# Kernel optimization log

Measured on AMD Instinct MI355X. Metric: run time of the kernel, lower is better.

Reference implementation:

```python
import jax, jax.numpy as jnp
import numpy as np

C, P, H, W, BS = 256, 2, 128, 128, 4
NH, DH = 16, 16
NPATCH = (H // P) * (W // P)   # 4096
NTOK = NPATCH + 1              # 4097 with cls token
NMASK = int((1 - 0.75) * NTOK) # 1024 kept (visible) tokens
PRED = 512
NUM_BLOCKS = 1

def _sincos_pos_embed(embed_dim, h, w):
    # faithful port of get_2d_sincos_pos_embed
    def emb1d(d, pos):
        omega = np.arange(d // 2, dtype=np.float64) / (d / 2.0)
        omega = 1.0 / 10000 ** omega
        out = np.einsum('m,d->md', pos.reshape(-1), omega)
        return np.concatenate([np.sin(out), np.cos(out)], axis=1)
    gh = np.arange(h, dtype=np.float32)
    gw = np.arange(w, dtype=np.float32)
    grid = np.stack(np.meshgrid(gw, gh), axis=0).reshape(2, 1, h, w)
    emb = np.concatenate([emb1d(embed_dim // 2, grid[0]), emb1d(embed_dim // 2, grid[1])], axis=1)
    return jnp.asarray(emb, jnp.float32)  # [h*w, embed_dim]

def _ln(x, g, b, eps=1e-5):
    mu = x.mean(-1, keepdims=True)
    var = ((x - mu) ** 2).mean(-1, keepdims=True)
    return (x - mu) * jax.lax.rsqrt(var + eps) * g + b

def _gelu(x):
    return jax.nn.gelu(x, approximate=False)  # torch nn.GELU default (erf)

def _attn(x, qkv_w, qkv_b, proj_w, proj_b, nq_g, nq_b, nk_g, nk_b):
    bs, n, c = x.shape
    qkv = x @ qkv_w + qkv_b
    q, k, v = jnp.split(qkv, 3, axis=-1)
    heads = lambda t: t.reshape(bs, n, NH, DH).transpose(0, 2, 1, 3)  # [b,h,n,d]
    q, k, v = heads(q), heads(k), heads(v)
    q = _ln(q, nq_g, nq_b)  # per-head-dim QK LayerNorm
    k = _ln(k, nk_g, nk_b)
    score = jnp.einsum('bhnd,bhmd->bhnm', q, k) / np.float32(np.sqrt(DH))
    attn = jax.nn.softmax(score, axis=-1)
    attn_map = attn.mean(axis=1)[:, 0, 1:]  # [b, n-1]
    out = jnp.einsum('bhnm,bhmd->bhnd', attn, v)
    out = out.transpose(0, 2, 1, 3).reshape(bs, n, c)
    return out @ proj_w + proj_b, attn_map

def _forward(mask_index, x, Wp, bp, cls, qkv_w, qkv_b, proj_w, proj_b, nq_g, nq_b, nk_g, nk_b,
             conv_w, conv_b, ca1_w, ca1_b, ca2_w, ca2_b, mlp1_w, mlp1_b, mlp2_w, mlp2_b,
             node_w, ln0_g, ln0_b, h1_w, h1_b, ln1_g, ln1_b, h2_w, h2_b, ln2_g, ln2_b,
             h3_w, h3_b, pr_w, pr_b):
    bs = x.shape[0]
    # PatchEmbed: conv stride=kernel=P expressed as reshape + einsum
    xp = x.reshape(bs, 3, H // P, P, W // P, P)
    tok = jnp.einsum('bchpwq,ocpq->bohw', xp, Wp) + bp[None, :, None, None]
    tok = tok.reshape(bs, C, NPATCH).transpose(0, 2, 1)  # [b, l, c]
    tok = tok + _sincos_pos_embed(C, H // P, W // P)[None]
    tok = jnp.concatenate([jnp.broadcast_to(cls, (bs, 1, C)), tok], axis=1)  # prepend cls
    # mask_img: keep NMASK tokens per the precomputed permutation prefix
    m = jnp.take_along_axis(tok, mask_index[:, :, None], axis=1)  # [b, NMASK, C]

    attn_map = None
    for blk in range(NUM_BLOCKS):
        feat = m[..., None]  # feature_list: [b, l, c, width]
        for i in range(4):
            j = blk * 4 + i
            xl = feat[..., -1]
            o1 = _gelu(xl @ conv_w[j] + conv_b[j])  # Conv1x1Act
            gate = jax.nn.sigmoid(jax.nn.relu(xl @ ca1_w[j] + ca1_b[j]) @ ca2_w[j] + ca2_b[j])
            o2 = gate * xl                           # ChannelAttention
            o4 = _gelu(xl @ mlp1_w[j] + mlp1_b[j]) @ mlp2_w[j] + mlp2_b[j]  # MLP
            cat = jnp.concatenate([feat, jnp.stack([o1, o2, xl, o4], axis=-1)], axis=-1)  # width 5+i
            wmix = jax.nn.softmax(node_w[j, :5 + i] / 0.01)
            mixed = jnp.einsum('blcn,n->blc', cat, wmix)
            a_out, attn_map = _attn(mixed, qkv_w[j], qkv_b[j], proj_w[j], proj_b[j],
                                    nq_g[j], nq_b[j], nk_g[j], nk_b[j])
            xo = a_out + mixed  # residual
            feat = jnp.concatenate([feat, xo[..., None]], axis=-1)
        m = xo
    # Predict_head (tokenwise)
    h = _ln(m, ln0_g, ln0_b)
    h = h @ h1_w + h1_b
    h = _ln(h, ln1_g, ln1_b)
    h = h @ h2_w + h2_b
    h = _ln(h, ln2_g, ln2_b)
    h = h @ h3_w + h3_b
    return h @ pr_w + pr_b  # [b, NMASK, PRED]

def setup_inputs():
    key = jax.random.key(0)
    ks = iter(jax.random.split(key, 64))
    rn = lambda shape, s=0.02: jax.random.normal(next(ks), shape, jnp.float32) * s
    noise = jax.random.normal(next(ks), (BS, NTOK))
    mask_index = jnp.argsort(noise, axis=-1)[:, :NMASK].astype(jnp.int32)
    return dict(
        x=jax.random.normal(next(ks), (BS, 3, H, W), jnp.float32),
        mask_index=mask_index,
        Wp=rn((C, 3, P, P)), bp=jnp.zeros((C,)), cls=rn((1, 1, C)),
        qkv_w=rn((4, C, 3 * C)), qkv_b=jnp.zeros((4, 3 * C)),
        proj_w=rn((4, C, C)), proj_b=jnp.zeros((4, C)),
        nq_g=jnp.ones((4, DH)), nq_b=jnp.zeros((4, DH)),
        nk_g=jnp.ones((4, DH)), nk_b=jnp.zeros((4, DH)),
        conv_w=rn((4, C, C)), conv_b=jnp.zeros((4, C)),
        ca1_w=rn((4, C, C // 16)), ca1_b=jnp.zeros((4, C // 16)),
        ca2_w=rn((4, C // 16, C)), ca2_b=jnp.zeros((4, C)),
        mlp1_w=rn((4, C, 4 * C)), mlp1_b=jnp.zeros((4, 4 * C)),
        mlp2_w=rn((4, 4 * C, C)), mlp2_b=jnp.zeros((4, C)),
        node_w=jax.random.normal(next(ks), (4, 8), jnp.float32),
        ln0_g=jnp.ones((C,)), ln0_b=jnp.zeros((C,)),
        h1_w=rn((C, 2048)), h1_b=jnp.zeros((2048,)),
        ln1_g=jnp.ones((2048,)), ln1_b=jnp.zeros((2048,)),
        h2_w=rn((2048, 256)), h2_b=jnp.zeros((256,)),
        ln2_g=jnp.ones((256,)), ln2_b=jnp.zeros((256,)),
        h3_w=rn((256, 2048)), h3_b=jnp.zeros((2048,)),
        pr_w=rn((2048, PRED)), pr_b=jnp.zeros((PRED,)),
    )

def reference(x, mask_index, Wp, bp, cls, qkv_w, qkv_b, proj_w, proj_b, nq_g, nq_b, nk_g, nk_b,
              conv_w, conv_b, ca1_w, ca1_b, ca2_w, ca2_b, mlp1_w, mlp1_b, mlp2_w, mlp2_b,
              node_w, ln0_g, ln0_b, h1_w, h1_b, ln1_g, ln1_b, h2_w, h2_b, ln2_g, ln2_b,
              h3_w, h3_b, pr_w, pr_b):
    return _forward(mask_index, x, Wp, bp, cls, qkv_w, qkv_b, proj_w, proj_b, nq_g, nq_b, nk_g, nk_b,
                    conv_w, conv_b, ca1_w, ca1_b, ca2_w, ca2_b, mlp1_w, mlp1_b, mlp2_w, mlp2_b,
                    node_w, ln0_g, ln0_b, h1_w, h1_b, ln1_g, ln1_b, h2_w, h2_b, ln2_g, ln2_b,
                    h3_w, h3_b, pr_w, pr_b)
```

## Files before the change

kernel.cpp:

```cpp
#include <hip/hip_runtime.h>
#include <math.h>
#include <cstddef>

#define RTOK 4096
#define CDIM 256
#define NHEAD 16
#define DHEAD 16
#define SEQ 1024
#define BSZ 4

#define ACT_NONE 0
#define ACT_GELU 1

typedef short short8 __attribute__((ext_vector_type(8)));
typedef float f32x4  __attribute__((ext_vector_type(4)));
typedef _Float16 half8 __attribute__((ext_vector_type(8)));
typedef _Float16 half4 __attribute__((ext_vector_type(4)));

__device__ __forceinline__ float gelu_erf(float x) {
    return 0.5f * x * (1.0f + erff(x * 0.70710678118654752f));
}
__device__ __forceinline__ unsigned short f2b(float f) {
    unsigned u = __float_as_uint(f);
    unsigned r = (u + 0x7FFFu + ((u >> 16) & 1u)) >> 16;
    return (unsigned short)r;
}
__device__ __forceinline__ float b2f(unsigned short u) {
    return __uint_as_float((unsigned)u << 16);
}
__device__ __forceinline__ void gld16(const unsigned short* g, unsigned short* l) {
    __builtin_amdgcn_global_load_lds(
        (const __attribute__((address_space(1))) unsigned int*)g,
        (__attribute__((address_space(3))) unsigned int*)l, 16, 0, 0);
}

struct WtSeg { const float* in; unsigned short* out; int K, N, ntx, tpz, zin, zout; };
struct WtTab { WtSeg s[9]; int cum[10]; };

__global__ __launch_bounds__(256) void wtrans_all(WtTab tab)
{
    int g = blockIdx.x;
    int si = 0;
    #pragma unroll
    for (int i = 0; i < 8; ++i) if (g >= tab.cum[i + 1]) si = i + 1;
    WtSeg sg = tab.s[si];
    int t = g - tab.cum[si];
    int z = t / sg.tpz, r = t % sg.tpz;
    int kb = (r % sg.ntx) * 32, nb = (r / sg.ntx) * 32;
    const float* in = sg.in + (size_t)z * sg.zin;
    unsigned short* out = sg.out + (size_t)z * sg.zout;

    __shared__ float tt[32][33];
    int tx = threadIdx.x & 31, ty = threadIdx.x >> 5;
    #pragma unroll
    for (int rr = 0; rr < 4; ++rr) {
        int kk = ty * 4 + rr;
        tt[kk][tx] = in[(size_t)(kb + kk) * sg.N + nb + tx];
    }
    __syncthreads();
    #pragma unroll
    for (int rr = 0; rr < 4; ++rr) {
        int nn = ty * 4 + rr;
        out[(size_t)(nb + nn) * sg.K + kb + tx] = f2b(tt[tx][nn]);
    }
}

__global__ __launch_bounds__(256) void embed_kernel(
    const float* __restrict__ x, const int* __restrict__ mask_index,
    const float* __restrict__ Wp, const float* __restrict__ bp,
    const float* __restrict__ cls,
    float* __restrict__ out, unsigned short* __restrict__ outb)
{
    int row = blockIdx.x;
    int b = row >> 10;
    int c = threadIdx.x;
    int idx = mask_index[row];
    if (idx == 0) {
        float v = cls[c];
        out[(size_t)row * 256 + c] = v;
        outb[(size_t)row * 256 + c] = f2b(v);
        return;
    }
    int p  = idx - 1;
    int ph = p >> 6, pw = p & 63;

    __shared__ float xs[12];
    if (c < 12) {
        int ch = c >> 2, r = (c >> 1) & 1, q = c & 1;
        xs[c] = x[(((size_t)b * 3 + ch) * 128 + (ph * 2 + r)) * 128 + (pw * 2 + q)];
    }
    __syncthreads();

    float acc = bp[c];
    #pragma unroll
    for (int t = 0; t < 12; ++t) acc += xs[t] * Wp[c * 12 + t];

    int part = c >> 6, cc = c & 63;
    double omega = exp((double)cc * -0.14391156831212787);
    double posv  = (part < 2) ? (double)pw : (double)ph;
    double a     = posv * omega;
    double e     = ((part & 1) == 0) ? sin(a) : cos(a);
    float v = acc + (float)e;
    out[(size_t)row * 256 + c] = v;
    outb[(size_t)row * 256 + c] = f2b(v);
}

template<int MT, int ACT, bool RES, bool FOUT, int BMODE, bool SPLIT>
__global__ __launch_bounds__(256) void gemm_mfma(
    const unsigned short* __restrict__ A, const unsigned short* __restrict__ Bt,
    const float* __restrict__ bias, const float* __restrict__ bias1,
    const float* __restrict__ Rsd,
    float* __restrict__ C, unsigned short* __restrict__ Cb,
    int M, int N, int K, int N0)
{
    constexpr int BM = 64 * MT;
    __shared__ __align__(16) unsigned short As[BM * 64];
    __shared__ __align__(16) unsigned short Bs[64 * 64];
    int tid = threadIdx.x;
    int w = tid >> 6, lane = tid & 63;
    int l15 = lane & 15, q = lane >> 4;

    int gx = gridDim.x, gy = gridDim.y;
    int L = blockIdx.x + gx * blockIdx.y;
    int xcd = L & 7, j = L >> 3;
    int by = xcd * (gy >> 3) + j / gx;
    int bx = j - (j / gx) * gx;
    int row0 = by * BM, col0 = bx * 64;

    f32x4 acc[MT][4];
    #pragma unroll
    for (int mt = 0; mt < MT; ++mt)
        #pragma unroll
        for (int nt = 0; nt < 4; ++nt)
            acc[mt][nt] = (f32x4){0.f, 0.f, 0.f, 0.f};

    for (int kb = 0; kb < K; kb += 64) {
        __syncthreads();
        #pragma unroll
        for (int t = 0; t < 2 * MT; ++t) {
            int slot = tid + t * 256;
            int r = slot >> 3;
            int s = (slot & 7) ^ (r & 7);
            gld16(A + (size_t)(row0 + r) * K + kb + s * 8, &As[slot * 8]);
        }
        #pragma unroll
        for (int t = 0; t < 2; ++t) {
            int slot = tid + t * 256;
            int r = slot >> 3;
            int s = (slot & 7) ^ (r & 7);
            gld16(Bt + (size_t)(col0 + r) * K + kb + s * 8, &Bs[slot * 8]);
        }
        __syncthreads();

        #pragma unroll
        for (int hh = 0; hh < 2; ++hh) {
            short8 af[MT];
            #pragma unroll
            for (int mt = 0; mt < MT; ++mt) {
                int R = w * 16 * MT + mt * 16 + l15;
                int c = hh * 4 + q;
                af[mt] = *(const short8*)&As[R * 64 + ((c ^ (R & 7)) << 3)];
            }
            #pragma unroll
            for (int nt = 0; nt < 4; ++nt) {
                int R = nt * 16 + l15;
                int c = hh * 4 + q;
                short8 bf = *(const short8*)&Bs[R * 64 + ((c ^ (R & 7)) << 3)];
                #pragma unroll
                for (int mt = 0; mt < MT; ++mt)
                    acc[mt][nt] = __builtin_amdgcn_mfma_f32_16x16x32_bf16(
                        af[mt], bf, acc[mt][nt], 0, 0, 0);
            }
        }
    }

    #pragma unroll
    for (int mt = 0; mt < MT; ++mt) {
        #pragma unroll
        for (int nt = 0; nt < 4; ++nt) {
            #pragma unroll
            for (int reg = 0; reg < 4; ++reg) {
                int row = row0 + w * 16 * MT + mt * 16 + q * 4 + reg;
                int col = col0 + nt * 16 + l15;
                if (SPLIT) {
                    float v = acc[mt][nt][reg] +
                              (col < N0 ? bias[col] : bias1[col - N0]);
                    if (ACT == ACT_GELU) v = gelu_erf(v);
                    if (col < N0) C[(size_t)row * N0 + col] = v;
                    else Cb[(size_t)row * (N - N0) + (col - N0)] = f2b(v);
                } else {
                    float v = acc[mt][nt][reg] + bias[col];
                    if (ACT == ACT_GELU) v = gelu_erf(v);
                    if (RES) v += Rsd[(size_t)row * N + col];
                    if (FOUT) C[(size_t)row * N + col] = v;
                    if (BMODE == 1) Cb[(size_t)row * N + col] = f2b(v);
                    if (BMODE == 2) {
                        _Float16 hv = (_Float16)v;
                        Cb[(size_t)row * N + col] = *(unsigned short*)&hv;
                    }
                }
            }
        }
    }
}

__global__ __launch_bounds__(256) void chanattn_kernel(
    const float* __restrict__ xl, const float* __restrict__ ca1w,
    const float* __restrict__ ca1b, const float* __restrict__ ca2w,
    const float* __restrict__ ca2b, float* __restrict__ o2)
{
    __shared__ float xs[256];
    __shared__ float sm16[16];
    size_t row = blockIdx.x;
    int tid = threadIdx.x;
    xs[tid] = xl[row * 256 + tid];
    __syncthreads();

    int h = tid >> 4, part = tid & 15;
    float p = 0.f;
    #pragma unroll
    for (int i = 0; i < 16; ++i)
        p += xs[part * 16 + i] * ca1w[(part * 16 + i) * 16 + h];
    p += __shfl_down(p, 8, 16);
    p += __shfl_down(p, 4, 16);
    p += __shfl_down(p, 2, 16);
    p += __shfl_down(p, 1, 16);
    if (part == 0) sm16[h] = fmaxf(p + ca1b[h], 0.0f);
    __syncthreads();

    float g = ca2b[tid];
    #pragma unroll
    for (int hh = 0; hh < 16; ++hh) g += sm16[hh] * ca2w[hh * 256 + tid];
    g = 1.0f / (1.0f + expf(-g));
    o2[row * 256 + tid] = g * xs[tid];
}

__global__ __launch_bounds__(256) void mix_kernel(
    const float* p0, const float* p1, const float* p2, const float* p3,
    const float* p4, const float* p5, const float* p6, const float* p7,
    const float* __restrict__ node_w, int cnt,
    float* __restrict__ out, unsigned short* __restrict__ outb, int n)
{
    int i = blockIdx.x * 256 + threadIdx.x;
    if (i >= n) return;
    float w[8];
    float mx = -1e30f;
    for (int t = 0; t < cnt; ++t) { w[t] = node_w[t] * 100.0f; mx = fmaxf(mx, w[t]); }
    float s = 0.0f;
    for (int t = 0; t < cnt; ++t) { w[t] = expf(w[t] - mx); s += w[t]; }
    float inv = 1.0f / s;
    const float* ps[8] = {p0, p1, p2, p3, p4, p5, p6, p7};
    float v = 0.0f;
    for (int t = 0; t < cnt; ++t) v += w[t] * inv * ps[t][i];
    out[i] = v;
    outb[i] = f2b(v);
}

__global__ __launch_bounds__(256) void ln256_kernel(
    const float* __restrict__ in, unsigned short* __restrict__ outb,
    const float* __restrict__ g, const float* __restrict__ bb)
{
    int row = blockIdx.x * 4 + (threadIdx.x >> 6);
    int lane = threadIdx.x & 63;
    f32x4 xv = *(const f32x4*)(in + (size_t)row * 256 + lane * 4);
    float s = xv[0] + xv[1] + xv[2] + xv[3];
    #pragma unroll
    for (int off = 1; off < 64; off <<= 1) s += __shfl_xor(s, off, 64);
    float mu = s * (1.0f / 256.0f);
    float d0 = xv[0]-mu, d1 = xv[1]-mu, d2 = xv[2]-mu, d3 = xv[3]-mu;
    float s2 = d0*d0 + d1*d1 + d2*d2 + d3*d3;
    #pragma unroll
    for (int off = 1; off < 64; off <<= 1) s2 += __shfl_xor(s2, off, 64);
    float rstd = rsqrtf(s2 * (1.0f / 256.0f) + 1e-5f);
    f32x4 gv = *(const f32x4*)(g + lane * 4);
    f32x4 bv = *(const f32x4*)(bb + lane * 4);
    ushort4 o;
    o.x = f2b(d0 * rstd * gv[0] + bv[0]);
    o.y = f2b(d1 * rstd * gv[1] + bv[1]);
    o.z = f2b(d2 * rstd * gv[2] + bv[2]);
    o.w = f2b(d3 * rstd * gv[3] + bv[3]);
    *(ushort4*)(outb + (size_t)row * 256 + lane * 4) = o;
}

__global__ __launch_bounds__(256) void lnwb_kernel(
    const unsigned short* __restrict__ in, unsigned short* __restrict__ outb,
    const float* __restrict__ g, const float* __restrict__ bb, int N)
{
    __shared__ float sm[4];
    size_t row = blockIdx.x;
    const unsigned short* xr = in + row * N;
    int lane = threadIdx.x & 63, wid = threadIdx.x >> 6;

    float s = 0.0f;
    for (int i = threadIdx.x; i < N; i += 256) s += b2f(xr[i]);
    #pragma unroll
    for (int off = 32; off > 0; off >>= 1) s += __shfl_down(s, off, 64);
    if (lane == 0) sm[wid] = s;
    __syncthreads();
    float mu = (sm[0] + sm[1] + sm[2] + sm[3]) / N;
    __syncthreads();

    float s2 = 0.0f;
    for (int i = threadIdx.x; i < N; i += 256) { float d = b2f(xr[i]) - mu; s2 += d * d; }
    #pragma unroll
    for (int off = 32; off > 0; off >>= 1) s2 += __shfl_down(s2, off, 64);
    if (lane == 0) sm[wid] = s2;
    __syncthreads();
    float var = (sm[0] + sm[1] + sm[2] + sm[3]) / N;
    float rstd = rsqrtf(var + 1e-5f);

    for (int i = threadIdx.x; i < N; i += 256)
        outb[row * N + i] = f2b((b2f(xr[i]) - mu) * rstd * g[i] + bb[i]);
}

__global__ __launch_bounds__(256) void attn_kernel(
    const unsigned short* __restrict__ qkvh,
    const float* __restrict__ nqg, const float* __restrict__ nqb,
    const float* __restrict__ nkg, const float* __restrict__ nkb,
    unsigned short* __restrict__ outb)
{
    int qt = blockIdx.x, h = blockIdx.y, b = blockIdx.z;
    int tid = threadIdx.x;
    int w = tid >> 6, lane = tid & 63;
    int l15 = lane & 15, quad = lane >> 4;
    const _Float16* qkv = (const _Float16*)qkvh;

    __shared__ __align__(16) _Float16 Qs[128 * 40];
    __shared__ __align__(16) _Float16 Kb[128 * 40];
    __shared__ __align__(16) _Float16 Vt[16 * 136];
    __shared__ __align__(16) _Float16 Ps[4][16 * 136];

    const float QSC = 0.25f * 1.44269504088896340736f;

    if (tid < 128) {
        int r = tid;
        const _Float16* qp = qkv + ((size_t)(b * 1024 + qt * 128 + r)) * 768 + h * 16;
        half8 a0 = *(const half8*)(qp);
        half8 a1 = *(const half8*)(qp + 8);
        float v[16];
        #pragma unroll
        for (int e = 0; e < 8; ++e) { v[e] = (float)a0[e]; v[8 + e] = (float)a1[e]; }
        float mu = 0.f;
        #pragma unroll
        for (int d = 0; d < 16; ++d) mu += v[d];
        mu *= (1.0f / 16.0f);
        float var = 0.f;
        #pragma unroll
        for (int d = 0; d < 16; ++d) { float t = v[d] - mu; var += t * t; }
        var *= (1.0f / 16.0f);
        float rstd = rsqrtf(var + 1e-5f);
        #pragma unroll
        for (int d4 = 0; d4 < 4; ++d4) {
            half4 t;
            #pragma unroll
            for (int e = 0; e < 4; ++e)
                t[e] = (_Float16)(((v[d4*4+e] - mu) * rstd * nqg[d4*4+e] + nqb[d4*4+e]) * QSC);
            *(half4*)&Qs[r * 40 + d4 * 4] = t;
        }
        half4 z = (half4){(_Float16)0, (_Float16)0, (_Float16)0, (_Float16)0};
        #pragma unroll
        for (int d4 = 4; d4 < 8; ++d4) {
            *(half4*)&Qs[r * 40 + d4 * 4] = z;
            *(half4*)&Kb[r * 40 + d4 * 4] = z;
        }
    }
    __syncthreads();

    half8 bq[2];
    bq[0] = *(const half8*)&Qs[(w * 32 + l15) * 40 + quad * 8];
    bq[1] = *(const half8*)&Qs[(w * 32 + 16 + l15) * 40 + quad * 8];

    float mst[2] = {-1e30f, -1e30f};
    float lst[2] = {0.f, 0.f};
    f32x4 acco[2];
    acco[0] = (f32x4){0.f, 0.f, 0.f, 0.f};
    acco[1] = (f32x4){0.f, 0.f, 0.f, 0.f};

    for (int kt = 0; kt < 8; ++kt) {
        __syncthreads();
        if (tid < 128) {
            int r = tid;
            const _Float16* kp = qkv + ((size_t)(b * 1024 + kt * 128 + r)) * 768 + 256 + h * 16;
            half8 a0 = *(const half8*)(kp);
            half8 a1 = *(const half8*)(kp + 8);
            float v[16];
            #pragma unroll
            for (int e = 0; e < 8; ++e) { v[e] = (float)a0[e]; v[8 + e] = (float)a1[e]; }
            float mu = 0.f;
            #pragma unroll
            for (int d = 0; d < 16; ++d) mu += v[d];
            mu *= (1.0f / 16.0f);
            float var = 0.f;
            #pragma unroll
            for (int d = 0; d < 16; ++d) { float t = v[d] - mu; var += t * t; }
            var *= (1.0f / 16.0f);
            float rstd = rsqrtf(var + 1e-5f);
            #pragma unroll
            for (int d4 = 0; d4 < 4; ++d4) {
                half4 t;
                #pragma unroll
                for (int e = 0; e < 4; ++e)
                    t[e] = (_Float16)((v[d4*4+e] - mu) * rstd * nkg[d4*4+e] + nkb[d4*4+e]);
                *(half4*)&Kb[r * 40 + d4 * 4] = t;
            }
        } else {
            int r = tid - 128;
            const _Float16* vp = qkv + ((size_t)(b * 1024 + kt * 128 + r)) * 768 + 512 + h * 16;
            half8 a0 = *(const half8*)(vp);
            half8 a1 = *(const half8*)(vp + 8);
            #pragma unroll
            for (int e = 0; e < 8; ++e) {
                Vt[e * 136 + r] = a0[e];
                Vt[(8 + e) * 136 + r] = a1[e];
            }
        }
        __syncthreads();

        f32x4 sacc[2][8];
        #pragma unroll
        for (int ni = 0; ni < 8; ++ni) {
            half8 ak = *(const half8*)&Kb[(ni * 16 + l15) * 40 + quad * 8];
            sacc[0][ni] = __builtin_amdgcn_mfma_f32_16x16x32_f16(
                ak, bq[0], (f32x4){0.f, 0.f, 0.f, 0.f}, 0, 0, 0);
            sacc[1][ni] = __builtin_amdgcn_mfma_f32_16x16x32_f16(
                ak, bq[1], (f32x4){0.f, 0.f, 0.f, 0.f}, 0, 0, 0);
        }

        half8 bv[4];
        #pragma unroll
        for (int c = 0; c < 4; ++c)
            bv[c] = *(const half8*)&Vt[l15 * 136 + c * 32 + quad * 8];

        #pragma unroll
        for (int mi = 0; mi < 2; ++mi) {
            float rm = sacc[mi][0][0];
            #pragma unroll
            for (int ni = 0; ni < 8; ++ni)
                #pragma unroll
                for (int reg = 0; reg < 4; ++reg)
                    rm = fmaxf(rm, sacc[mi][ni][reg]);
            rm = fmaxf(rm, __shfl_xor(rm, 16, 64));
            rm = fmaxf(rm, __shfl_xor(rm, 32, 64));
            float mn  = fmaxf(mst[mi], rm);
            float cor = exp2f(mst[mi] - mn);
            mst[mi] = mn;
            lst[mi] *= cor;
            #pragma unroll
            for (int reg = 0; reg < 4; ++reg) {
                float cR = __shfl(cor, (lane & 48) + quad * 4 + reg, 64);
                acco[mi][reg] *= cR;
            }
            float lsum = 0.f;
            #pragma unroll
            for (int ni = 0; ni < 8; ++ni) {
                half4 ph;
                #pragma unroll
                for (int reg = 0; reg < 4; ++reg) {
                    float p = exp2f(sacc[mi][ni][reg] - mn);
                    lsum += p;
                    ph[reg] = (_Float16)p;
                }
                *(half4*)&Ps[w][l15 * 136 + ni * 16 + quad * 4] = ph;
            }
            lsum += __shfl_xor(lsum, 16, 64);
            lsum += __shfl_xor(lsum, 32, 64);
            lst[mi] += lsum;

            #pragma unroll
            for (int c = 0; c < 4; ++c) {
                half8 p0 = *(const half8*)&Ps[w][l15 * 136 + c * 32 + quad * 8];
                acco[mi] = __builtin_amdgcn_mfma_f32_16x16x32_f16(p0, bv[c], acco[mi], 0, 0, 0);
            }
        }
    }

    #pragma unroll
    for (int mi = 0; mi < 2; ++mi) {
        #pragma unroll
        for (int reg = 0; reg < 4; ++reg) {
            float lR = __shfl(lst[mi], (lane & 48) + quad * 4 + reg, 64);
            float o = acco[mi][reg] / lR;
            int row = b * 1024 + qt * 128 + w * 32 + mi * 16 + quad * 4 + reg;
            outb[(size_t)row * 256 + h * 16 + l15] = f2b(o);
        }
    }
}

extern "C" void kernel_launch(void* const* d_in, const int* in_sizes, int n_in,
                              void* d_out, int out_size, void* d_ws, size_t ws_size,
                              hipStream_t stream)
{
    const float* x          = (const float*)d_in[0];
    const int*   mask_index = (const int*)  d_in[1];
    const float* Wp         = (const float*)d_in[2];
    const float* bp         = (const float*)d_in[3];
    const float* cls        = (const float*)d_in[4];
    const float* qkv_w      = (const float*)d_in[5];
    const float* qkv_b      = (const float*)d_in[6];
    const float* proj_w     = (const float*)d_in[7];
    const float* proj_b     = (const float*)d_in[8];
    const float* nq_g       = (const float*)d_in[9];
    const float* nq_b       = (const float*)d_in[10];
    const float* nk_g       = (const float*)d_in[11];
    const float* nk_b       = (const float*)d_in[12];
    const float* conv_w     = (const float*)d_in[13];
    const float* conv_b     = (const float*)d_in[14];
    const float* ca1_w      = (const float*)d_in[15];
    const float* ca1_b      = (const float*)d_in[16];
    const float* ca2_w      = (const float*)d_in[17];
    const float* ca2_b      = (const float*)d_in[18];
    const float* mlp1_w     = (const float*)d_in[19];
    const float* mlp1_b     = (const float*)d_in[20];
    const float* mlp2_w     = (const float*)d_in[21];
    const float* mlp2_b     = (const float*)d_in[22];
    const float* node_w     = (const float*)d_in[23];
    const float* ln0_g      = (const float*)d_in[24];
    const float* ln0_b      = (const float*)d_in[25];
    const float* h1_w       = (const float*)d_in[26];
    const float* h1_b       = (const float*)d_in[27];
    const float* ln1_g      = (const float*)d_in[28];
    const float* ln1_b      = (const float*)d_in[29];
    const float* h2_w       = (const float*)d_in[30];
    const float* h2_b       = (const float*)d_in[31];
    const float* ln2_g      = (const float*)d_in[32];
    const float* ln2_b      = (const float*)d_in[33];
    const float* h3_w       = (const float*)d_in[34];
    const float* h3_b       = (const float*)d_in[35];
    const float* pr_w       = (const float*)d_in[36];
    const float* pr_b       = (const float*)d_in[37];
    float* out = (float*)d_out;

    char* base = (char*)d_ws;
    size_t off = 0;
    auto alloc = [&](size_t bytes) -> char* {
        char* p = base + off;
        off += (bytes + 255) & ~(size_t)255;
        return p;
    };
    const size_t RC = (size_t)RTOK * CDIM;
    float* F[5];
    unsigned short* Fb[5];
    for (int i = 0; i < 5; ++i) F[i] = (float*)alloc(RC * 4);
    for (int i = 0; i < 5; ++i) Fb[i] = (unsigned short*)alloc(RC * 2);
    float* O1  = (float*)alloc(RC * 4);
    float* O2  = (float*)alloc(RC * 4);
    float* O4  = (float*)alloc(RC * 4);
    float* MIX = (float*)alloc(RC * 4);
    unsigned short* MIXb = (unsigned short*)alloc(RC * 2);
    unsigned short* AOb  = (unsigned short*)alloc(RC * 2);
    unsigned short* BIGH = (unsigned short*)alloc((size_t)RTOK * 768 * 2);
    unsigned short* H1b  = (unsigned short*)alloc((size_t)RTOK * 2048 * 2);
    unsigned short* MIDU = (unsigned short*)alloc((size_t)RTOK * 2048 * 2);
    unsigned short* L0b  = (unsigned short*)alloc(RC * 2);
    unsigned short* L2b  = (unsigned short*)alloc(RC * 2);
    unsigned short* H3b  = (unsigned short*)alloc((size_t)RTOK * 2048 * 2);
    unsigned short* cm1b  = (unsigned short*)alloc((size_t)4 * 1280 * 256 * 2);
    unsigned short* qkvb  = (unsigned short*)alloc((size_t)4 * 768 * 256 * 2);
    unsigned short* projb = (unsigned short*)alloc((size_t)4 * 256 * 256 * 2);
    unsigned short* mlp2b = (unsigned short*)alloc((size_t)4 * 256 * 1024 * 2);
    unsigned short* h1b   = (unsigned short*)alloc((size_t)2048 * 256 * 2);
    unsigned short* h2b   = (unsigned short*)alloc((size_t)256 * 2048 * 2);
    unsigned short* h3b   = (unsigned short*)alloc((size_t)2048 * 256 * 2);
    unsigned short* prb   = (unsigned short*)alloc((size_t)512 * 2048 * 2);

    {
        WtTab tab;
        int c = 0, idx = 0;
        auto seg = [&](const float* in, unsigned short* outp, int K, int N,
                       int z, int zin, int zout) {
            WtSeg s; s.in = in; s.out = outp; s.K = K; s.N = N;
            s.ntx = K / 32; s.tpz = (K / 32) * (N / 32);
            s.zin = zin; s.zout = zout;
            tab.s[idx] = s; tab.cum[idx] = c;
            c += s.tpz * z; ++idx;
        };
        seg(conv_w, cm1b,         256, 256,  4, 256 * 256,  1280 * 256);
        seg(mlp1_w, cm1b + 65536, 256, 1024, 4, 256 * 1024, 1280 * 256);
        seg(qkv_w,  qkvb,  256, 768,  4, 256 * 768,  768 * 256);
        seg(proj_w, projb, 256, 256,  4, 256 * 256,  256 * 256);
        seg(mlp2_w, mlp2b, 1024, 256, 4, 1024 * 256, 256 * 1024);
        seg(h1_w, h1b, 256, 2048, 1, 0, 0);
        seg(h2_w, h2b, 2048, 256, 1, 0, 0);
        seg(h3_w, h3b, 256, 2048, 1, 0, 0);
        seg(pr_w, prb, 2048, 512, 1, 0, 0);
        tab.cum[9] = c;
        wtrans_all<<<c, 256, 0, stream>>>(tab);
    }

    embed_kernel<<<RTOK, 256, 0, stream>>>(x, mask_index, Wp, bp, cls, F[0], Fb[0]);

    for (int j = 0; j < 4; ++j) {
        const float* xl = F[j];
        const unsigned short* xlb = Fb[j];
        gemm_mfma<2, ACT_GELU, false, false, 0, true><<<dim3(20, 32), 256, 0, stream>>>(
            xlb, cm1b + (size_t)j * 1280 * 256, conv_b + j * 256, mlp1_b + j * 1024,
            nullptr, O1, MIDU, RTOK, 1280, 256, 256);
        chanattn_kernel<<<RTOK, 256, 0, stream>>>(
            xl, ca1_w + (size_t)j * 256 * 16, ca1_b + j * 16,
            ca2_w + (size_t)j * 16 * 256, ca2_b + j * 256, O2);
        gemm_mfma<1, ACT_NONE, false, true, 0, false><<<dim3(4, 64), 256, 0, stream>>>(
            MIDU, mlp2b + (size_t)j * 256 * 1024, mlp2_b + j * 256, nullptr, nullptr,
            O4, nullptr, RTOK, 256, 1024, 0);
        const float* ps[8] = {nullptr, nullptr, nullptr, nullptr,
                              nullptr, nullptr, nullptr, nullptr};
        int cnt = 0;
        for (int t = 0; t <= j; ++t) ps[cnt++] = F[t];
        ps[cnt++] = O1; ps[cnt++] = O2; ps[cnt++] = F[j]; ps[cnt++] = O4;
        mix_kernel<<<(int)(RC / 256), 256, 0, stream>>>(
            ps[0], ps[1], ps[2], ps[3], ps[4], ps[5], ps[6], ps[7],
            node_w + j * 8, cnt, MIX, MIXb, (int)RC);
        gemm_mfma<2, ACT_NONE, false, false, 2, false><<<dim3(12, 32), 256, 0, stream>>>(
            MIXb, qkvb + (size_t)j * 768 * 256, qkv_b + j * 768, nullptr, nullptr,
            nullptr, BIGH, RTOK, 768, 256, 0);
        attn_kernel<<<dim3(8, NHEAD, BSZ), 256, 0, stream>>>(
            BIGH, nq_g + j * 16, nq_b + j * 16, nk_g + j * 16, nk_b + j * 16, AOb);
        gemm_mfma<1, ACT_NONE, true, true, 1, false><<<dim3(4, 64), 256, 0, stream>>>(
            AOb, projb + (size_t)j * 256 * 256, proj_b + j * 256, nullptr, MIX,
            F[j + 1], Fb[j + 1], RTOK, 256, 256, 0);
    }

    ln256_kernel<<<1024, 256, 0, stream>>>(F[4], L0b, ln0_g, ln0_b);
    gemm_mfma<2, ACT_NONE, false, false, 1, false><<<dim3(32, 32), 256, 0, stream>>>(
        L0b, h1b, h1_b, nullptr, nullptr, nullptr, H1b, RTOK, 2048, 256, 0);
    lnwb_kernel<<<RTOK, 256, 0, stream>>>(H1b, MIDU, ln1_g, ln1_b, 2048);
    gemm_mfma<1, ACT_NONE, false, true, 0, false><<<dim3(4, 64), 256, 0, stream>>>(
        MIDU, h2b, h2_b, nullptr, nullptr, MIX, nullptr, RTOK, 256, 2048, 0);
    ln256_kernel<<<1024, 256, 0, stream>>>(MIX, L2b, ln2_g, ln2_b);
    gemm_mfma<2, ACT_NONE, false, false, 1, false><<<dim3(32, 32), 256, 0, stream>>>(
        L2b, h3b, h3_b, nullptr, nullptr, nullptr, H3b, RTOK, 2048, 256, 0);
    gemm_mfma<1, ACT_NONE, false, true, 0, false><<<dim3(8, 64), 256, 0, stream>>>(
        H3b, prb, pr_b, nullptr, nullptr, out, nullptr, RTOK, 512, 2048, 0);
}
```

Measured before the change: 735.7 us.

## Fuse node-weighted mixing into GEMM epilogues and split attention preprocessing

```diff
diff --git a/kernel.cpp b/kernel.cpp
--- a/kernel.cpp
+++ b/kernel.cpp
@@ -32,6 +32,14 @@
     __builtin_amdgcn_global_load_lds(
         (const __attribute__((address_space(1))) unsigned int*)g,
         (__attribute__((address_space(3))) unsigned int*)l, 16, 0, 0);
+}
+__device__ __forceinline__ float node_wsel(const float* nwp, int cnt, int widx) {
+    float ww[8];
+    float mx = -1e30f;
+    for (int t = 0; t < cnt; ++t) { ww[t] = nwp[t] * 100.0f; mx = fmaxf(mx, ww[t]); }
+    float ssum = 0.0f;
+    for (int t = 0; t < cnt; ++t) { ww[t] = expf(ww[t] - mx); ssum += ww[t]; }
+    return ww[widx] / ssum;
 }
 
 struct WtSeg { const float* in; unsigned short* out; int K, N, ntx, tpz, zin, zout; };
@@ -105,13 +113,14 @@
     outb[(size_t)row * 256 + c] = f2b(v);
 }
 
-template<int MT, int ACT, bool RES, bool FOUT, int BMODE, bool SPLIT>
+template<int MT, int ACT, bool RES, bool FOUT, int BMODE, bool SPLIT, int NW>
 __global__ __launch_bounds__(256) void gemm_mfma(
     const unsigned short* __restrict__ A, const unsigned short* __restrict__ Bt,
     const float* __restrict__ bias, const float* __restrict__ bias1,
     const float* __restrict__ Rsd,
     float* __restrict__ C, unsigned short* __restrict__ Cb,
-    int M, int N, int K, int N0)
+    int M, int N, int K, int N0,
+    const float* __restrict__ nwp, int ncnt, int widx)
 {
     constexpr int BM = 64 * MT;
     __shared__ __align__(16) unsigned short As[BM * 64];
@@ -174,6 +183,9 @@
         }
     }
 
+    float wsel = 0.0f;
+    if (NW > 0) wsel = node_wsel(nwp, ncnt, widx);
+
     #pragma unroll
     for (int mt = 0; mt < MT; ++mt) {
         #pragma unroll
@@ -186,12 +198,17 @@
                     float v = acc[mt][nt][reg] +
                               (col < N0 ? bias[col] : bias1[col - N0]);
                     if (ACT == ACT_GELU) v = gelu_erf(v);
-                    if (col < N0) C[(size_t)row * N0 + col] = v;
-                    else Cb[(size_t)row * (N - N0) + (col - N0)] = f2b(v);
+                    if (col < N0) {
+                        if (NW == 1) C[(size_t)row * N0 + col] += wsel * v;
+                        else         C[(size_t)row * N0 + col] = v;
+                    } else {
+                        Cb[(size_t)row * (N - N0) + (col - N0)] = f2b(v);
+                    }
                 } else {
                     float v = acc[mt][nt][reg] + bias[col];
                     if (ACT == ACT_GELU) v = gelu_erf(v);
-                    if (RES) v += Rsd[(size_t)row * N + col];
+                    if (NW == 2) v = wsel * v + Rsd[(size_t)row * N + col];
+                    else if (RES) v += Rsd[(size_t)row * N + col];
                     if (FOUT) C[(size_t)row * N + col] = v;
                     if (BMODE == 1) Cb[(size_t)row * N + col] = f2b(v);
                     if (BMODE == 2) {
@@ -205,9 +222,12 @@
 }
 
 __global__ __launch_bounds__(256) void chanattn_kernel(
-    const float* __restrict__ xl, const float* __restrict__ ca1w,
-    const float* __restrict__ ca1b, const float* __restrict__ ca2w,
-    const float* __restrict__ ca2b, float* __restrict__ o2)
+    const float* __restrict__ xl,
+    const float* f0, const float* f1, const float* f2,
+    const float* __restrict__ ca1w, const float* __restrict__ ca1b,
+    const float* __restrict__ ca2w, const float* __restrict__ ca2b,
+    const float* __restrict__ node_w, int cnt,
+    float* __restrict__ MIX)
 {
     __shared__ float xs[256];
     __shared__ float sm16[16];
@@ -232,28 +252,19 @@
     #pragma unroll
     for (int hh = 0; hh < 16; ++hh) g += sm16[hh] * ca2w[hh * 256 + tid];
     g = 1.0f / (1.0f + expf(-g));
-    o2[row * 256 + tid] = g * xs[tid];
-}
-
-__global__ __launch_bounds__(256) void mix_kernel(
-    const float* p0, const float* p1, const float* p2, const float* p3,
-    const float* p4, const float* p5, const float* p6, const float* p7,
-    const float* __restrict__ node_w, int cnt,
-    float* __restrict__ out, unsigned short* __restrict__ outb, int n)
-{
-    int i = blockIdx.x * 256 + threadIdx.x;
-    if (i >= n) return;
-    float w[8];
+    float o2 = g * xs[tid];
+
+    float ww[8];
     float mx = -1e30f;
-    for (int t = 0; t < cnt; ++t) { w[t] = node_w[t] * 100.0f; mx = fmaxf(mx, w[t]); }
-    float s = 0.0f;
-    for (int t = 0; t < cnt; ++t) { w[t] = expf(w[t] - mx); s += w[t]; }
-    float inv = 1.0f / s;
-    const float* ps[8] = {p0, p1, p2, p3, p4, p5, p6, p7};
-    float v = 0.0f;
-    for (int t = 0; t < cnt; ++t) v += w[t] * inv * ps[t][i];
-    out[i] = v;
-    outb[i] = f2b(v);
+    for (int t = 0; t < cnt; ++t) { ww[t] = node_w[t] * 100.0f; mx = fmaxf(mx, ww[t]); }
+    float ssum = 0.0f;
+    for (int t = 0; t < cnt; ++t) { ww[t] = expf(ww[t] - mx); ssum += ww[t]; }
+    float inv = 1.0f / ssum;
+    int j = cnt - 5;
+    float acc = (ww[j] + ww[j + 3]) * inv * xs[tid] + ww[j + 2] * inv * o2;
+    const float* fs[3] = {f0, f1, f2};
+    for (int t = 0; t < j; ++t) acc += ww[t] * inv * fs[t][row * 256 + tid];
+    MIX[row * 256 + tid] = acc;
 }
 
 __global__ __launch_bounds__(256) void ln256_kernel(
@@ -313,176 +324,206 @@
         outb[row * N + i] = f2b((b2f(xr[i]) - mu) * rstd * g[i] + bb[i]);
 }
 
-__global__ __launch_bounds__(256) void attn_kernel(
+__global__ __launch_bounds__(256) void attn_prep(
     const unsigned short* __restrict__ qkvh,
     const float* __restrict__ nqg, const float* __restrict__ nqb,
     const float* __restrict__ nkg, const float* __restrict__ nkb,
+    unsigned short* __restrict__ Qph, unsigned short* __restrict__ Kph,
+    unsigned short* __restrict__ Vph)
+{
+    int b = blockIdx.x >> 6;
+    int tokbase = (blockIdx.x & 63) * 16;
+    int tid = threadIdx.x;
+    int tl = tid >> 4, h = tid & 15;
+    int tok = tokbase + tl;
+    const _Float16* qkv = (const _Float16*)qkvh;
+    const _Float16* rowp = qkv + ((size_t)(b * 1024 + tok)) * 768;
+    _Float16* Qp = (_Float16*)Qph;
+    _Float16* Kp = (_Float16*)Kph;
+    _Float16* Vp = (_Float16*)Vph;
+    const float QSC = 0.25f * 1.44269504088896340736f;
+
+    __shared__ _Float16 vt[16][16][17];
+
+    {
+        half8 a0 = *(const half8*)(rowp + h * 16);
+        half8 a1 = *(const half8*)(rowp + h * 16 + 8);
+        float v[16];
+        #pragma unroll
+        for (int e = 0; e < 8; ++e) { v[e] = (float)a0[e]; v[8 + e] = (float)a1[e]; }
+        float mu = 0.f;
+        #pragma unroll
+        for (int d = 0; d < 16; ++d) mu += v[d];
+        mu *= (1.0f / 16.0f);
+        float var = 0.f;
+        #pragma unroll
+        for (int d = 0; d < 16; ++d) { float t = v[d] - mu; var += t * t; }
+        var *= (1.0f / 16.0f);
+        float rstd = rsqrtf(var + 1e-5f);
+        half8 o0, o1;
+        #pragma unroll
+        for (int e = 0; e < 8; ++e) {
+            o0[e] = (_Float16)(((v[e] - mu) * rstd * nqg[e] + nqb[e]) * QSC);
+            o1[e] = (_Float16)(((v[8+e] - mu) * rstd * nqg[8+e] + nqb[8+e]) * QSC);
+        }
+        _Float16* qo = Qp + ((size_t)(b * 16 + h) * 1024 + tok) * 16;
+        *(half8*)qo = o0;
+        *(half8*)(qo + 8) = o1;
+    }
+    {
+        half8 a0 = *(const half8*)(rowp + 256 + h * 16);
+        half8 a1 = *(const half8*)(rowp + 256 + h * 16 + 8);
+        float v[16];
+        #pragma unroll
+        for (int e = 0; e < 8; ++e) { v[e] = (float)a0[e]; v[8 + e] = (float)a1[e]; }
+        float mu = 0.f;
+        #pragma unroll
+        for (int d = 0; d < 16; ++d) mu += v[d];
+        mu *= (1.0f / 16.0f);
+        float var = 0.f;
+        #pragma unroll
+        for (int d = 0; d < 16; ++d) { float t = v[d] - mu; var += t * t; }
+        var *= (1.0f / 16.0f);
+        float rstd = rsqrtf(var + 1e-5f);
+        half8 o0, o1;
+        #pragma unroll
+        for (int e = 0; e < 8; ++e) {
+            o0[e] = (_Float16)((v[e] - mu) * rstd * nkg[e] + nkb[e]);
+            o1[e] = (_Float16)((v[8+e] - mu) * rstd * nkg[8+e] + nkb[8+e]);
+        }
+        _Float16* ko = Kp + ((size_t)(b * 16 + h) * 1024 + tok) * 16;
+        *(half8*)ko = o0;
+        *(half8*)(ko + 8) = o1;
+    }
+    {
+        half8 a0 = *(const half8*)(rowp + 512 + h * 16);
+        half8 a1 = *(const half8*)(rowp + 512 + h * 16 + 8);
+        #pragma unroll
+        for (int e = 0; e < 8; ++e) { vt[tl][h][e] = a0[e]; vt[tl][h][8 + e] = a1[e]; }
+    }
+    __syncthreads();
+    {
+        int h2 = tid >> 4, d = tid & 15;
+        half8 o0, o1;
+        #pragma unroll
+        for (int t = 0; t < 8; ++t) { o0[t] = vt[t][h2][d]; o1[t] = vt[8 + t][h2][d]; }
+        _Float16* vo = Vp + ((size_t)(b * 16 + h2) * 16 + d) * 1024 + tokbase;
+        *(half8*)vo = o0;
+        *(half8*)(vo + 8) = o1;
+    }
+}
+
+__global__ __launch_bounds__(256) void attn_kernel(
+    const unsigned short* __restrict__ Qph, const unsigned short* __restrict__ Kph,
+    const unsigned short* __restrict__ Vph,
     unsigned short* __restrict__ outb)
 {
     int qt = blockIdx.x, h = blockIdx.y, b = blockIdx.z;
+    int bh = b * 16 + h;
     int tid = threadIdx.x;
     int w = tid >> 6, lane = tid & 63;
     int l15 = lane & 15, quad = lane >> 4;
-    const _Float16* qkv = (const _Float16*)qkvh;
-
-    __shared__ __align__(16) _Float16 Qs[128 * 40];
+    const _Float16* Qp = (const _Float16*)Qph + (size_t)bh * 1024 * 16;
+    const _Float16* Kp = (const _Float16*)Kph + (size_t)bh * 1024 * 16;
+    const _Float16* Vp = (const _Float16*)Vph + (size_t)bh * 16 * 1024;
+
+    __shared__ __align__(16) _Float16 Qs[64 * 40];
     __shared__ __align__(16) _Float16 Kb[128 * 40];
     __shared__ __align__(16) _Float16 Vt[16 * 136];
     __shared__ __align__(16) _Float16 Ps[4][16 * 136];
 
-    const float QSC = 0.25f * 1.44269504088896340736f;
-
+    uint4 z4 = {0, 0, 0, 0};
+    if (tid < 64) {
+        *(uint4*)&Qs[tid * 40 + 16] = z4;
+        *(uint4*)&Qs[tid * 40 + 24] = z4;
+    } else if (tid < 192) {
+        int r = tid - 64;
+        *(uint4*)&Kb[r * 40 + 16] = z4;
+        *(uint4*)&Kb[r * 40 + 24] = z4;
+    }
     if (tid < 128) {
-        int r = tid;
-        const _Float16* qp = qkv + ((size_t)(b * 1024 + qt * 128 + r)) * 768 + h * 16;
-        half8 a0 = *(const half8*)(qp);
-        half8 a1 = *(const half8*)(qp + 8);
-        float v[16];
-        #pragma unroll
-        for (int e = 0; e < 8; ++e) { v[e] = (float)a0[e]; v[8 + e] = (float)a1[e]; }
-        float mu = 0.f;
-        #pragma unroll
-        for (int d = 0; d < 16; ++d) mu += v[d];
-        mu *= (1.0f / 16.0f);
-        float var = 0.f;
-        #pragma unroll
-        for (int d = 0; d < 16; ++d) { float t = v[d] - mu; var += t * t; }
-        var *= (1.0f / 16.0f);
-        float rstd = rsqrtf(var + 1e-5f);
-        #pragma unroll
-        for (int d4 = 0; d4 < 4; ++d4) {
-            half4 t;
-            #pragma unroll
-            for (int e = 0; e < 4; ++e)
-                t[e] = (_Float16)(((v[d4*4+e] - mu) * rstd * nqg[d4*4+e] + nqb[d4*4+e]) * QSC);
-            *(half4*)&Qs[r * 40 + d4 * 4] = t;
-        }
-        half4 z = (half4){(_Float16)0, (_Float16)0, (_Float16)0, (_Float16)0};
-        #pragma unroll
-        for (int d4 = 4; d4 < 8; ++d4) {
-            *(half4*)&Qs[r * 40 + d4 * 4] = z;
-            *(half4*)&Kb[r * 40 + d4 * 4] = z;
-        }
-    }
-    __syncthreads();
-
-    half8 bq[2];
-    bq[0] = *(const half8*)&Qs[(w * 32 + l15) * 40 + quad * 8];
-    bq[1] = *(const half8*)&Qs[(w * 32 + 16 + l15) * 40 + quad * 8];
-
-    float mst[2] = {-1e30f, -1e30f};
-    float lst[2] = {0.f, 0.f};
-    f32x4 acco[2];
-    acco[0] = (f32x4){0.f, 0.f, 0.f, 0.f};
-    acco[1] = (f32x4){0.f, 0.f, 0.f, 0.f};
+        int r = tid >> 1, part = tid & 1;
+        *(uint4*)&Qs[r * 40 + part * 8] =
+            *(const uint4*)(Qp + (size_t)(qt * 64 + r) * 16 + part * 8);
+    }
+    __syncthreads();
+
+    half8 bq = *(const half8*)&Qs[(w * 16 + l15) * 40 + quad * 8];
+    float mst = -1e30f, lst = 0.f;
+    f32x4 acco = (f32x4){0.f, 0.f, 0.f, 0.f};
 
     for (int kt = 0; kt < 8; ++kt) {
         __syncthreads();
-        if (tid < 128) {
-            int r = tid;
-            const _Float16* kp = qkv + ((size_t)(b * 1024 + kt * 128 + r)) * 768 + 256 + h * 16;
-            half8 a0 = *(const half8*)(kp);
-            half8 a1 = *(const half8*)(kp + 8);
-            float v[16];
-            #pragma unroll
-            for (int e = 0; e < 8; ++e) { v[e] = (float)a0[e]; v[8 + e] = (float)a1[e]; }
-            float mu = 0.f;
-            #pragma unroll
-            for (int d = 0; d < 16; ++d) mu += v[d];
-            mu *= (1.0f / 16.0f);
-            float var = 0.f;
-            #pragma unroll
-            for (int d = 0; d < 16; ++d) { float t = v[d] - mu; var += t * t; }
-            var *= (1.0f / 16.0f);
-            float rstd = rsqrtf(var + 1e-5f);
-            #pragma unroll
-            for (int d4 = 0; d4 < 4; ++d4) {
-                half4 t;
-                #pragma unroll
-                for (int e = 0; e < 4; ++e)
-                    t[e] = (_Float16)((v[d4*4+e] - mu) * rstd * nkg[d4*4+e] + nkb[d4*4+e]);
-                *(half4*)&Kb[r * 40 + d4 * 4] = t;
-            }
-        } else {
-            int r = tid - 128;
-            const _Float16* vp = qkv + ((size_t)(b * 1024 + kt * 128 + r)) * 768 + 512 + h * 16;
-            half8 a0 = *(const half8*)(vp);
-            half8 a1 = *(const half8*)(vp + 8);
-            #pragma unroll
-            for (int e = 0; e < 8; ++e) {
-                Vt[e * 136 + r] = a0[e];
-                Vt[(8 + e) * 136 + r] = a1[e];
-            }
+        {
+            int r = tid >> 1, part = tid & 1;
+            *(uint4*)&Kb[r * 40 + part * 8] =
+                *(const uint4*)(Kp + (size_t)(kt * 128 + r) * 16 + part * 8);
+        }
+        {
+            int d = tid >> 4, kk8 = tid & 15;
+            *(uint4*)&Vt[d * 136 + kk8 * 8] =
+                *(const uint4*)(Vp + (size_t)d * 1024 + kt * 128 + kk8 * 8);
         }
         __syncthreads();
 
-        f32x4 sacc[2][8];
+        f32x4 sacc[8];
         #pragma unroll
         for (int ni = 0; ni < 8; ++ni) {
             half8 ak = *(const half8*)&Kb[(ni * 16 + l15) * 40 + quad * 8];
-            sacc[0][ni] = __builtin_amdgcn_mfma_f32_16x16x32_f16(
-                ak, bq[0], (f32x4){0.f, 0.f, 0.f, 0.f}, 0, 0, 0);
-            sacc[1][ni] = __builtin_amdgcn_mfma_f32_16x16x32_f16(
-                ak, bq[1], (f32x4){0.f, 0.f, 0.f, 0.f}, 0, 0, 0);
-        }
-
+            sacc[ni] = __builtin_amdgcn_mfma_f32_16x16x32_f16(
+                ak, bq, (f32x4){0.f, 0.f, 0.f, 0.f}, 0, 0, 0);
+        }
         half8 bv[4];
         #pragma unroll
         for (int c = 0; c < 4; ++c)
             bv[c] = *(const half8*)&Vt[l15 * 136 + c * 32 + quad * 8];
 
-        #pragma unroll
-        for (int mi = 0; mi < 2; ++mi) {
-            float rm = sacc[mi][0][0];
+        float rm = sacc[0][0];
+        #pragma unroll
+        for (int ni = 0; ni < 8; ++ni)
             #pragma unroll
-            for (int ni = 0; ni < 8; ++ni)
-                #pragma unroll
-                for (int reg = 0; reg < 4; ++reg)
-                    rm = fmaxf(rm, sacc[mi][ni][reg]);
-            rm = fmaxf(rm, __shfl_xor(rm, 16, 64));
-            rm = fmaxf(rm, __shfl_xor(rm, 32, 64));
-            float mn  = fmaxf(mst[mi], rm);
-            float cor = exp2f(mst[mi] - mn);
-            mst[mi] = mn;
-            lst[mi] *= cor;
+            for (int reg = 0; reg < 4; ++reg)
+                rm = fmaxf(rm, sacc[ni][reg]);
+        rm = fmaxf(rm, __shfl_xor(rm, 16, 64));
+        rm = fmaxf(rm, __shfl_xor(rm, 32, 64));
+        float mn  = fmaxf(mst, rm);
+        float cor = exp2f(mst - mn);
+        mst = mn;
+        lst *= cor;
+        #pragma unroll
+        for (int reg = 0; reg < 4; ++reg) {
+            float cR = __shfl(cor, (lane & 48) + quad * 4 + reg, 64);
+            acco[reg] *= cR;
+        }
+        float lsum = 0.f;
+        #pragma unroll
+        for (int ni = 0; ni < 8; ++ni) {
+            half4 ph;
             #pragma unroll
             for (int reg = 0; reg < 4; ++reg) {
-                float cR = __shfl(cor, (lane & 48) + quad * 4 + reg, 64);
-                acco[mi][reg] *= cR;
+                float p = exp2f(sacc[ni][reg] - mn);
+                lsum += p;
+                ph[reg] = (_Float16)p;
             }
-            float lsum = 0.f;
-            #pragma unroll
-            for (int ni = 0; ni < 8; ++ni) {
-                half4 ph;
-                #pragma unroll
-                for (int reg = 0; reg < 4; ++reg) {
-                    float p = exp2f(sacc[mi][ni][reg] - mn);
-                    lsum += p;
-                    ph[reg] = (_Float16)p;
-                }
-                *(half4*)&Ps[w][l15 * 136 + ni * 16 + quad * 4] = ph;
-            }
-            lsum += __shfl_xor(lsum, 16, 64);
-            lsum += __shfl_xor(lsum, 32, 64);
-            lst[mi] += lsum;
-
-            #pragma unroll
-            for (int c = 0; c < 4; ++c) {
-                half8 p0 = *(const half8*)&Ps[w][l15 * 136 + c * 32 + quad * 8];
-                acco[mi] = __builtin_amdgcn_mfma_f32_16x16x32_f16(p0, bv[c], acco[mi], 0, 0, 0);
-            }
-        }
-    }
-
-    #pragma unroll
-    for (int mi = 0; mi < 2; ++mi) {
-        #pragma unroll
-        for (int reg = 0; reg < 4; ++reg) {
-            float lR = __shfl(lst[mi], (lane & 48) + quad * 4 + reg, 64);
-            float o = acco[mi][reg] / lR;
-            int row = b * 1024 + qt * 128 + w * 32 + mi * 16 + quad * 4 + reg;
-            outb[(size_t)row * 256 + h * 16 + l15] = f2b(o);
-        }
+            *(half4*)&Ps[w][l15 * 136 + ni * 16 + quad * 4] = ph;
+        }
+        lsum += __shfl_xor(lsum, 16, 64);
+        lsum += __shfl_xor(lsum, 32, 64);
+        lst += lsum;
+
+        #pragma unroll
+        for (int c = 0; c < 4; ++c) {
+            half8 p0 = *(const half8*)&Ps[w][l15 * 136 + c * 32 + quad * 8];
+            acco = __builtin_amdgcn_mfma_f32_16x16x32_f16(p0, bv[c], acco, 0, 0, 0);
+        }
+    }
+
+    #pragma unroll
+    for (int reg = 0; reg < 4; ++reg) {
+        float lR = __shfl(lst, (lane & 48) + quad * 4 + reg, 64);
+        float o = acco[reg] / lR;
+        int row = b * 1024 + qt * 64 + w * 16 + quad * 4 + reg;
+        outb[(size_t)row * 256 + h * 16 + l15] = f2b(o);
     }
 }
 
@@ -542,13 +583,13 @@
     unsigned short* Fb[5];
     for (int i = 0; i < 5; ++i) F[i] = (float*)alloc(RC * 4);
     for (int i = 0; i < 5; ++i) Fb[i] = (unsigned short*)alloc(RC * 2);
-    float* O1  = (float*)alloc(RC * 4);
-    float* O2  = (float*)alloc(RC * 4);
-    float* O4  = (float*)alloc(RC * 4);
     float* MIX = (float*)alloc(RC * 4);
     unsigned short* MIXb = (unsigned short*)alloc(RC * 2);
     unsigned short* AOb  = (unsigned short*)alloc(RC * 2);
     unsigned short* BIGH = (unsigned short*)alloc((size_t)RTOK * 768 * 2);
+    unsigned short* Qp   = (unsigned short*)alloc((size_t)RTOK * 256 * 2);
+    unsigned short* Kp   = (unsigned short*)alloc((size_t)RTOK * 256 * 2);
+    unsigned short* Vp   = (unsigned short*)alloc((size_t)RTOK * 256 * 2);
     unsigned short* H1b  = (unsigned short*)alloc((size_t)RTOK * 2048 * 2);
     unsigned short* MIDU = (unsigned short*)alloc((size_t)RTOK * 2048 * 2);
     unsigned short* L0b  = (unsigned short*)alloc(RC * 2);
@@ -592,42 +633,42 @@
     for (int j = 0; j < 4; ++j) {
         const float* xl = F[j];
         const unsigned short* xlb = Fb[j];
-        gemm_mfma<2, ACT_GELU, false, false, 0, true><<<dim3(20, 32), 256, 0, stream>>>(
+        chanattn_kernel<<<RTOK, 256, 0, stream>>>(
+            xl, F[0], F[1], F[2],
+            ca1_w + (size_t)j * 256 * 16, ca1_b + j * 16,
+            ca2_w + (size_t)j * 16 * 256, ca2_b + j * 256,
+            node_w + j * 8, 5 + j, MIX);
+        gemm_mfma<2, ACT_GELU, false, false, 0, true, 1><<<dim3(20, 32), 256, 0, stream>>>(
             xlb, cm1b + (size_t)j * 1280 * 256, conv_b + j * 256, mlp1_b + j * 1024,
-            nullptr, O1, MIDU, RTOK, 1280, 256, 256);
-        chanattn_kernel<<<RTOK, 256, 0, stream>>>(
-            xl, ca1_w + (size_t)j * 256 * 16, ca1_b + j * 16,
-            ca2_w + (size_t)j * 16 * 256, ca2_b + j * 256, O2);
-        gemm_mfma<1, ACT_NONE, false, true, 0, false><<<dim3(4, 64), 256, 0, stream>>>(
-            MIDU, mlp2b + (size_t)j * 256 * 1024, mlp2_b + j * 256, nullptr, nullptr,
-            O4, nullptr, RTOK, 256, 1024, 0);
-        const float* ps[8] = {nullptr, nullptr, nullptr, nullptr,
-                              nullptr, nullptr, nullptr, nullptr};
-        int cnt = 0;
-        for (int t = 0; t <= j; ++t) ps[cnt++] = F[t];
-        ps[cnt++] = O1; ps[cnt++] = O2; ps[cnt++] = F[j]; ps[cnt++] = O4;
-        mix_kernel<<<(int)(RC / 256), 256, 0, stream>>>(
-            ps[0], ps[1], ps[2], ps[3], ps[4], ps[5], ps[6], ps[7],
-            node_w + j * 8, cnt, MIX, MIXb, (int)RC);
-        gemm_mfma<2, ACT_NONE, false, false, 2, false><<<dim3(12, 32), 256, 0, stream>>>(
+            nullptr, MIX, MIDU, RTOK, 1280, 256, 256, node_w + j * 8, 5 + j, j + 1);
+        gemm_mfma<1, ACT_NONE, false, true, 1, false, 2><<<dim3(4, 64), 256, 0, stream>>>(
+            MIDU, mlp2b + (size_t)j * 256 * 1024, mlp2_b + j * 256, nullptr, MIX,
+            MIX, MIXb, RTOK, 256, 1024, 0, node_w + j * 8, 5 + j, j + 4);
+        gemm_mfma<2, ACT_NONE, false, false, 2, false, 0><<<dim3(12, 32), 256, 0, stream>>>(
             MIXb, qkvb + (size_t)j * 768 * 256, qkv_b + j * 768, nullptr, nullptr,
-            nullptr, BIGH, RTOK, 768, 256, 0);
-        attn_kernel<<<dim3(8, NHEAD, BSZ), 256, 0, stream>>>(
-            BIGH, nq_g + j * 16, nq_b + j * 16, nk_g + j * 16, nk_b + j * 16, AOb);
-        gemm_mfma<1, ACT_NONE, true, true, 1, false><<<dim3(4, 64), 256, 0, stream>>>(
+            nullptr, BIGH, RTOK, 768, 256, 0, nullptr, 0, 0);
+        attn_prep<<<256, 256, 0, stream>>>(
+            BIGH, nq_g + j * 16, nq_b + j * 16, nk_g + j * 16, nk_b + j * 16,
+            Qp, Kp, Vp);
+        attn_kernel<<<dim3(16, NHEAD, BSZ), 256, 0, stream>>>(Qp, Kp, Vp, AOb);
+        gemm_mfma<1, ACT_NONE, true, true, 1, false, 0><<<dim3(4, 64), 256, 0, stream>>>(
             AOb, projb + (size_t)j * 256 * 256, proj_b + j * 256, nullptr, MIX,
-            F[j + 1], Fb[j + 1], RTOK, 256, 256, 0);
+            F[j + 1], Fb[j + 1], RTOK, 256, 256, 0, nullptr, 0, 0);
     }
 
     ln256_kernel<<<1024, 256, 0, stream>>>(F[4], L0b, ln0_g, ln0_b);
-    gemm_mfma<2, ACT_NONE, false, false, 1, false><<<dim3(32, 32), 256, 0, stream>>>(
-        L0b, h1b, h1_b, nullptr, nullptr, nullptr, H1b, RTOK, 2048, 256, 0);
+    gemm_mfma<2, ACT_NONE, false, false, 1, false, 0><<<dim3(32, 32), 256, 0, stream>>>(
+        L0b, h1b, h1_b, nullptr, nullptr, nullptr, H1b, RTOK, 2048, 256, 0,
+        nullptr, 0, 0);
     lnwb_kernel<<<RTOK, 256, 0, stream>>>(H1b, MIDU, ln1_g, ln1_b, 2048);
-    gemm_mfma<1, ACT_NONE, false, true, 0, false><<<dim3(4, 64), 256, 0, stream>>>(
-        MIDU, h2b, h2_b, nullptr, nullptr, MIX, nullptr, RTOK, 256, 2048, 0);
+    gemm_mfma<1, ACT_NONE, false, true, 0, false, 0><<<dim3(4, 64), 256, 0, stream>>>(
+        MIDU, h2b, h2_b, nullptr, nullptr, MIX, nullptr, RTOK, 256, 2048, 0,
+        nullptr, 0, 0);
     ln256_kernel<<<1024, 256, 0, stream>>>(MIX, L2b, ln2_g, ln2_b);
-    gemm_mfma<2, ACT_NONE, false, false, 1, false><<<dim3(32, 32), 256, 0, stream>>>(
-        L2b, h3b, h3_b, nullptr, nullptr, nullptr, H3b, RTOK, 2048, 256, 0);
-    gemm_mfma<1, ACT_NONE, false, true, 0, false><<<dim3(8, 64), 256, 0, stream>>>(
-        H3b, prb, pr_b, nullptr, nullptr, out, nullptr, RTOK, 512, 2048, 0);
-}
+    gemm_mfma<2, ACT_NONE, false, false, 1, false, 0><<<dim3(32, 32), 256, 0, stream>>>(
+        L2b, h3b, h3_b, nullptr, nullptr, nullptr, H3b, RTOK, 2048, 256, 0,
+        nullptr, 0, 0);
+    gemm_mfma<1, ACT_NONE, false, true, 0, false, 0><<<dim3(8, 64), 256, 0, stream>>>(
+        H3b, prb, pr_b, nullptr, nullptr, out, nullptr, RTOK, 512, 2048, 0,
+        nullptr, 0, 0);
+}
```

Result: faster. 717.0 us (-2.5%).
